# Kernel optimization log

Hardware: AMD Instinct MI355X
Metric: run time of the kernel (lower is better)

Reference implementation:

```python
import jax, jax.numpy as jnp
import numpy as np

BLOCK_SIZE = 128
FP8_MAX = 448.0
IN_FEATURES = 4096
OUT_FEATURES = 4096


def _fp8_round(x):
    # Simulate float8_e4m3fn storage; fall back to clamp-only if dtype unsupported.
    try:
        return x.astype(jnp.float8_e4m3fn).astype(jnp.float32)
    except Exception:
        return x


def setup_inputs() -> dict:
    key = jax.random.key(0)
    kx, kw = jax.random.split(key)
    x = jax.random.normal(kx, (2, 4096, IN_FEATURES), dtype=jnp.float32)
    # Kaiming-uniform-ish init, then block-quantize exactly as fp8_block_quantize does.
    bound = 1.0 / np.sqrt(IN_FEATURES)
    w = jax.random.uniform(kw, (OUT_FEATURES, IN_FEATURES), minval=-bound, maxval=bound, dtype=jnp.float32)
    w_blocks = w.reshape(-1, BLOCK_SIZE)  # (n_blocks, 128); 4096*4096 divisible by 128
    block_abs_max = jnp.maximum(jnp.max(jnp.abs(w_blocks), axis=-1), 1e-12)
    fp8_scales = block_abs_max / FP8_MAX  # (n_blocks,)
    w_scaled = jnp.clip(w_blocks / fp8_scales[:, None], -FP8_MAX, FP8_MAX)
    weight_q = _fp8_round(w_scaled).reshape(OUT_FEATURES, IN_FEATURES)
    bias = jnp.zeros((OUT_FEATURES,), dtype=jnp.float32)
    return {"x": x, "weight_q": weight_q, "fp8_scales": fp8_scales, "bias": bias}


def reference(x, weight_q, fp8_scales, bias):
    # Block-wise dequantize: flatten weight, scale each 128-element block.
    w_blocks = weight_q.reshape(-1, BLOCK_SIZE)            # (n_blocks, 128)
    w = (w_blocks * fp8_scales[:, None]).reshape(OUT_FEATURES, IN_FEATURES)
    # F.linear: y = x @ w.T + b
    return jnp.einsum('bsk,nk->bsn', x, w) + bias
```

## Files before the change

kernel.cpp:

```cpp
#include <hip/hip_runtime.h>


#define M_DIM 8192
#define N_DIM 4096
#define K_DIM 4096
#define K_TILES (K_DIM / 64)

typedef short s16x8 __attribute__((ext_vector_type(8)));
typedef float f32x4 __attribute__((ext_vector_type(4)));

__device__ __forceinline__ unsigned short f32_to_bf16(float f) {
    unsigned int u = __float_as_uint(f);
    unsigned int r = (u + 0x7fffu + ((u >> 16) & 1u)) >> 16;
    return (unsigned short)r;
}

__device__ __forceinline__ ushort4 pack4(float4 a) {
    ushort4 r;
    r.x = f32_to_bf16(a.x); r.y = f32_to_bf16(a.y);
    r.z = f32_to_bf16(a.z); r.w = f32_to_bf16(a.w);
    return r;
}

__global__ __launch_bounds__(256) void cvt_fused_kernel(
    const float4* __restrict__ x, const float4* __restrict__ wq,
    const float* __restrict__ scales,
    ushort4* __restrict__ xo, ushort4* __restrict__ wo) {
    const int b = blockIdx.x;
    const int t = threadIdx.x;
    if (b < 16384) {
        const int base = b * 512 + t;
#pragma unroll
        for (int j = 0; j < 2; ++j) {
            const int idx = base + j * 256;
            xo[idx] = pack4(x[idx]);
        }
    } else {
        const int base = (b - 16384) * 512 + t;
#pragma unroll
        for (int j = 0; j < 2; ++j) {
            const int idx = base + j * 256;
            const float s = scales[idx >> 5];
            float4 a = wq[idx];
            a.x *= s; a.y *= s; a.z *= s; a.w *= s;
            wo[idx] = pack4(a);
        }
    }
}

__device__ __forceinline__ void async_copy16(const void* g, void* l) {
    __builtin_amdgcn_global_load_lds(
        (const __attribute__((address_space(1))) unsigned int*)g,
        (__attribute__((address_space(3))) unsigned int*)l,
        16, 0, 0);
}


#define STAGE_A_HALF(h, ktt, bufb) do {                                        \
    const unsigned short* g_ = gA0 + (ktt) * 64 + (h) * (64 * K_DIM);          \
    async_copy16(g_,               ldsA + (bufb) + (h) * 8192 + aOff);         \
    async_copy16(g_ + 128 * K_DIM, ldsA + (bufb) + (h) * 8192 + 16384 + aOff); \
  } while (0)

#define STAGE_B_HALF(h, ktt, bufb) do {                                        \
    const unsigned short* g_ = gB0 + (ktt) * 64 + (h) * (32 * K_DIM);          \
    async_copy16(g_,               ldsB + (bufb) + (h) * 4096 + bOff);         \
    async_copy16(g_ + 128 * K_DIM, ldsB + (bufb) + (h) * 4096 + 16384 + bOff); \
  } while (0)

#define PHASE(qm, qn, bufb, STAGE_STMT, WAITN) do {                            \
    STAGE_STMT;                                                                \
    asm volatile("s_waitcnt vmcnt(" #WAITN ")" ::: "memory");                  \
    __builtin_amdgcn_s_barrier();                                              \
    asm volatile("" ::: "memory");                                             \
    __builtin_amdgcn_sched_barrier(0);                                         \
    s16x8 af[4][2], bf[2][2];                                                  \
    _Pragma("unroll")                                                          \
    for (int i = 0; i < 4; ++i) {                                              \
      af[i][0] = *(const s16x8*)(ldsA + (bufb) + aRowB + ((qm)*64 + i*16)*128 + kk0); \
      af[i][1] = *(const s16x8*)(ldsA + (bufb) + aRowB + ((qm)*64 + i*16)*128 + kk1); \
    }                                                                          \
    _Pragma("unroll")                                                          \
    for (int j = 0; j < 2; ++j) {                                              \
      bf[j][0] = *(const s16x8*)(ldsB + (bufb) + bRowB + ((qn)*32 + j*16)*128 + kk0); \
      bf[j][1] = *(const s16x8*)(ldsB + (bufb) + bRowB + ((qn)*32 + j*16)*128 + kk1); \
    }                                                                          \
    __builtin_amdgcn_s_setprio(1);                                             \
    _Pragma("unroll")                                                          \
    for (int i = 0; i < 4; ++i)                                                \
      _Pragma("unroll")                                                        \
      for (int j = 0; j < 2; ++j) {                                            \
        acc[(qm)*4+i][(qn)*2+j] = __builtin_amdgcn_mfma_f32_16x16x32_bf16(     \
            af[i][0], bf[j][0], acc[(qm)*4+i][(qn)*2+j], 0, 0, 0);             \
        acc[(qm)*4+i][(qn)*2+j] = __builtin_amdgcn_mfma_f32_16x16x32_bf16(     \
            af[i][1], bf[j][1], acc[(qm)*4+i][(qn)*2+j], 0, 0, 0);             \
      }                                                                        \
    __builtin_amdgcn_s_setprio(0);                                             \
  } while (0)

__global__ __launch_bounds__(512, 2) void gemm_bt_kernel(
    const unsigned short* __restrict__ A,
    const unsigned short* __restrict__ B,
    const float* __restrict__ bias,
    float* __restrict__ C)
{
    __shared__ __align__(16) char lds[131072];
    char* ldsA = lds;
    char* ldsB = lds + 32768;

    const int t = threadIdx.x;
    const int l = t & 63;
    const int w = t >> 6;
    const int wr = w >> 2;
    const int wc = w & 3;

    int id = blockIdx.x;
    id = (id & 7) * 64 + (id >> 3);
    const int m0 = (id >> 4) * 256;
    const int n0 = (id & 15) * 256;

    const int trow = t >> 3;
    const int tcol = ((t & 7) * 8) ^ ((trow & 7) * 8);
    const unsigned short* gA0 = A + (long)(m0 + trow) * K_DIM + tcol;
    const int brow = ((t >> 8) * 64) + ((t & 255) >> 3);
    const unsigned short* gB0 = B + (long)(n0 + brow) * K_DIM + tcol;
    const int aOff = t * 16;
    const int bOff = ((t >> 8) * 8192) + ((t & 255) * 16);

    const int aRowB = (wr * 128 + (l & 15)) * 128;
    const int bRowB = (wc * 64  + (l & 15)) * 128;
    const int kx  = (l >> 4) * 16;
    const int sw  = (l & 7) * 16;
    const int kk0 = kx ^ sw;
    const int kk1 = (64 + kx) ^ sw;

    f32x4 acc[8][4] = {};

    STAGE_A_HALF(0, 0, 0);
    STAGE_B_HALF(0, 0, 0);
    STAGE_B_HALF(1, 0, 0);
    STAGE_A_HALF(1, 0, 0);

    for (int kt = 0; kt < K_TILES - 1; ++kt) {
        const int cb = (kt & 1) * 65536;
        const int nb = 65536 - cb;
        PHASE(0, 0, cb, STAGE_A_HALF(0, kt + 1, nb), 6);
        PHASE(0, 1, cb, STAGE_B_HALF(0, kt + 1, nb), 6);
        PHASE(1, 0, cb, STAGE_B_HALF(1, kt + 1, nb), 6);
        PHASE(1, 1, cb, STAGE_A_HALF(1, kt + 1, nb), 6);
    }
    {
        const int cb = ((K_TILES - 1) & 1) * 65536;
        PHASE(0, 0, cb, (void)0, 4);
        PHASE(0, 1, cb, (void)0, 2);
        PHASE(1, 0, cb, (void)0, 0);
        PHASE(1, 1, cb, (void)0, 0);
    }

    const int q4 = (l >> 4) * 4;
#pragma unroll
    for (int nf = 0; nf < 4; ++nf) {
        const int col = n0 + wc * 64 + nf * 16 + (l & 15);
        const float bv = bias[col];
#pragma unroll
        for (int mf = 0; mf < 8; ++mf) {
            const long row = m0 + wr * 128 + mf * 16 + q4;
#pragma unroll
            for (int r = 0; r < 4; ++r) {
                C[(row + r) * N_DIM + col] = acc[mf][nf][r] + bv;
            }
        }
    }
}

extern "C" void kernel_launch(void* const* d_in, const int* in_sizes, int n_in,
                              void* d_out, int out_size, void* d_ws, size_t ws_size,
                              hipStream_t stream) {
    const float* x      = (const float*)d_in[0];
    const float* wq     = (const float*)d_in[1];
    const float* scales = (const float*)d_in[2];
    const float* bias   = (const float*)d_in[3];
    float* out = (float*)d_out;

    unsigned short* x_bf = (unsigned short*)d_ws;
    unsigned short* w_bf = x_bf + (size_t)M_DIM * K_DIM;

    cvt_fused_kernel<<<24576, 256, 0, stream>>>(
        (const float4*)x, (const float4*)wq, scales,
        (ushort4*)x_bf, (ushort4*)w_bf);

    gemm_bt_kernel<<<dim3(512), dim3(512), 0, stream>>>(x_bf, w_bf, bias, out);
}
```

Baseline: 510.1 us.

## Restructure GEMM k-loop into two phases and use grid-stride 16B conversion

```diff
diff --git a/kernel.cpp b/kernel.cpp
--- a/kernel.cpp
+++ b/kernel.cpp
@@ -8,42 +8,42 @@
 
 typedef short s16x8 __attribute__((ext_vector_type(8)));
 typedef float f32x4 __attribute__((ext_vector_type(4)));
-
-__device__ __forceinline__ unsigned short f32_to_bf16(float f) {
-    unsigned int u = __float_as_uint(f);
-    unsigned int r = (u + 0x7fffu + ((u >> 16) & 1u)) >> 16;
-    return (unsigned short)r;
-}
-
-__device__ __forceinline__ ushort4 pack4(float4 a) {
-    ushort4 r;
-    r.x = f32_to_bf16(a.x); r.y = f32_to_bf16(a.y);
-    r.z = f32_to_bf16(a.z); r.w = f32_to_bf16(a.w);
-    return r;
+typedef unsigned int u32x4 __attribute__((ext_vector_type(4)));
+
+__device__ __forceinline__ unsigned int pack2_bf16(float a, float b) {
+    unsigned int ua = __float_as_uint(a);
+    unsigned int ub = __float_as_uint(b);
+    unsigned int ra = ((ua + 0x7fffu + ((ua >> 16) & 1u)) >> 16) & 0xffffu;
+    unsigned int rb = (ub + 0x7fffu + ((ub >> 16) & 1u)) & 0xffff0000u;
+    return ra | rb;
 }
 
 __global__ __launch_bounds__(256) void cvt_fused_kernel(
     const float4* __restrict__ x, const float4* __restrict__ wq,
     const float* __restrict__ scales,
-    ushort4* __restrict__ xo, ushort4* __restrict__ wo) {
-    const int b = blockIdx.x;
-    const int t = threadIdx.x;
-    if (b < 16384) {
-        const int base = b * 512 + t;
-#pragma unroll
-        for (int j = 0; j < 2; ++j) {
-            const int idx = base + j * 256;
-            xo[idx] = pack4(x[idx]);
-        }
-    } else {
-        const int base = (b - 16384) * 512 + t;
-#pragma unroll
-        for (int j = 0; j < 2; ++j) {
-            const int idx = base + j * 256;
-            const float s = scales[idx >> 5];
-            float4 a = wq[idx];
+    u32x4* __restrict__ xo, u32x4* __restrict__ wo) {
+    const int NX   = (M_DIM * K_DIM) / 8;
+    const int NTOT = NX + (N_DIM * K_DIM) / 8;
+    const int stride = gridDim.x * blockDim.x;
+    for (int u = blockIdx.x * blockDim.x + threadIdx.x; u < NTOT; u += stride) {
+        if (u < NX) {
+            const float4 a = x[2 * u];
+            const float4 b = x[2 * u + 1];
+            u32x4 r;
+            r[0] = pack2_bf16(a.x, a.y); r[1] = pack2_bf16(a.z, a.w);
+            r[2] = pack2_bf16(b.x, b.y); r[3] = pack2_bf16(b.z, b.w);
+            xo[u] = r;
+        } else {
+            const int v = u - NX;
+            const float s = scales[v >> 4];
+            float4 a = wq[2 * v];
+            float4 b = wq[2 * v + 1];
             a.x *= s; a.y *= s; a.z *= s; a.w *= s;
-            wo[idx] = pack4(a);
+            b.x *= s; b.y *= s; b.z *= s; b.w *= s;
+            u32x4 r;
+            r[0] = pack2_bf16(a.x, a.y); r[1] = pack2_bf16(a.z, a.w);
+            r[2] = pack2_bf16(b.x, b.y); r[3] = pack2_bf16(b.z, b.w);
+            wo[v] = r;
         }
     }
 }
@@ -68,33 +68,41 @@
     async_copy16(g_ + 128 * K_DIM, ldsB + (bufb) + (h) * 4096 + 16384 + bOff); \
   } while (0)
 
-#define PHASE(qm, qn, bufb, STAGE_STMT, WAITN) do {                            \
-    STAGE_STMT;                                                                \
-    asm volatile("s_waitcnt vmcnt(" #WAITN ")" ::: "memory");                  \
-    __builtin_amdgcn_s_barrier();                                              \
-    asm volatile("" ::: "memory");                                             \
-    __builtin_amdgcn_sched_barrier(0);                                         \
-    s16x8 af[4][2], bf[2][2];                                                  \
+#define READ_AF(dst, qm, bufb) do {                                            \
     _Pragma("unroll")                                                          \
-    for (int i = 0; i < 4; ++i) {                                              \
-      af[i][0] = *(const s16x8*)(ldsA + (bufb) + aRowB + ((qm)*64 + i*16)*128 + kk0); \
-      af[i][1] = *(const s16x8*)(ldsA + (bufb) + aRowB + ((qm)*64 + i*16)*128 + kk1); \
+    for (int i_ = 0; i_ < 4; ++i_) {                                           \
+      dst[i_][0] = *(const s16x8*)(ldsA + (bufb) + aRowB + ((qm)*64 + i_*16)*128 + kk0); \
+      dst[i_][1] = *(const s16x8*)(ldsA + (bufb) + aRowB + ((qm)*64 + i_*16)*128 + kk1); \
     }                                                                          \
+  } while (0)
+
+#define READ_BF(dst, qn, bufb) do {                                            \
     _Pragma("unroll")                                                          \
-    for (int j = 0; j < 2; ++j) {                                              \
-      bf[j][0] = *(const s16x8*)(ldsB + (bufb) + bRowB + ((qn)*32 + j*16)*128 + kk0); \
-      bf[j][1] = *(const s16x8*)(ldsB + (bufb) + bRowB + ((qn)*32 + j*16)*128 + kk1); \
+    for (int j_ = 0; j_ < 2; ++j_) {                                           \
+      dst[j_][0] = *(const s16x8*)(ldsB + (bufb) + bRowB + ((qn)*32 + j_*16)*128 + kk0); \
+      dst[j_][1] = *(const s16x8*)(ldsB + (bufb) + bRowB + ((qn)*32 + j_*16)*128 + kk1); \
     }                                                                          \
+  } while (0)
+
+#define MFMA32(qm, AF, BX, BY) do {                                            \
     __builtin_amdgcn_s_setprio(1);                                             \
     _Pragma("unroll")                                                          \
-    for (int i = 0; i < 4; ++i)                                                \
+    for (int i_ = 0; i_ < 4; ++i_) {                                           \
       _Pragma("unroll")                                                        \
-      for (int j = 0; j < 2; ++j) {                                            \
-        acc[(qm)*4+i][(qn)*2+j] = __builtin_amdgcn_mfma_f32_16x16x32_bf16(     \
-            af[i][0], bf[j][0], acc[(qm)*4+i][(qn)*2+j], 0, 0, 0);             \
-        acc[(qm)*4+i][(qn)*2+j] = __builtin_amdgcn_mfma_f32_16x16x32_bf16(     \
-            af[i][1], bf[j][1], acc[(qm)*4+i][(qn)*2+j], 0, 0, 0);             \
+      for (int j_ = 0; j_ < 2; ++j_) {                                         \
+        acc[(qm)*4+i_][j_] = __builtin_amdgcn_mfma_f32_16x16x32_bf16(          \
+            AF[i_][0], BX[j_][0], acc[(qm)*4+i_][j_], 0, 0, 0);                \
+        acc[(qm)*4+i_][j_] = __builtin_amdgcn_mfma_f32_16x16x32_bf16(          \
+            AF[i_][1], BX[j_][1], acc[(qm)*4+i_][j_], 0, 0, 0);                \
       }                                                                        \
+      _Pragma("unroll")                                                        \
+      for (int j_ = 0; j_ < 2; ++j_) {                                         \
+        acc[(qm)*4+i_][2+j_] = __builtin_amdgcn_mfma_f32_16x16x32_bf16(        \
+            AF[i_][0], BY[j_][0], acc[(qm)*4+i_][2+j_], 0, 0, 0);              \
+        acc[(qm)*4+i_][2+j_] = __builtin_amdgcn_mfma_f32_16x16x32_bf16(        \
+            AF[i_][1], BY[j_][1], acc[(qm)*4+i_][2+j_], 0, 0, 0);              \
+      }                                                                        \
+    }                                                                          \
     __builtin_amdgcn_s_setprio(0);                                             \
   } while (0)
 
@@ -135,6 +143,7 @@
     const int kk1 = (64 + kx) ^ sw;
 
     f32x4 acc[8][4] = {};
+    s16x8 af[4][2], bfX[2][2], bfY[2][2];
 
     STAGE_A_HALF(0, 0, 0);
     STAGE_B_HALF(0, 0, 0);
@@ -144,17 +153,35 @@
     for (int kt = 0; kt < K_TILES - 1; ++kt) {
         const int cb = (kt & 1) * 65536;
         const int nb = 65536 - cb;
-        PHASE(0, 0, cb, STAGE_A_HALF(0, kt + 1, nb), 6);
-        PHASE(0, 1, cb, STAGE_B_HALF(0, kt + 1, nb), 6);
-        PHASE(1, 0, cb, STAGE_B_HALF(1, kt + 1, nb), 6);
-        PHASE(1, 1, cb, STAGE_A_HALF(1, kt + 1, nb), 6);
+        STAGE_A_HALF(0, kt + 1, nb);
+        STAGE_B_HALF(0, kt + 1, nb);
+        asm volatile("s_waitcnt vmcnt(4)" ::: "memory");
+        __builtin_amdgcn_s_barrier();
+        __builtin_amdgcn_sched_barrier(0);
+        READ_AF(af, 0, cb);
+        READ_BF(bfX, 0, cb);
+        READ_BF(bfY, 1, cb);
+        MFMA32(0, af, bfX, bfY);
+        STAGE_B_HALF(1, kt + 1, nb);
+        STAGE_A_HALF(1, kt + 1, nb);
+        __builtin_amdgcn_s_barrier();
+        __builtin_amdgcn_sched_barrier(0);
+        READ_AF(af, 1, cb);
+        MFMA32(1, af, bfX, bfY);
     }
     {
         const int cb = ((K_TILES - 1) & 1) * 65536;
-        PHASE(0, 0, cb, (void)0, 4);
-        PHASE(0, 1, cb, (void)0, 2);
-        PHASE(1, 0, cb, (void)0, 0);
-        PHASE(1, 1, cb, (void)0, 0);
+        asm volatile("s_waitcnt vmcnt(0)" ::: "memory");
+        __builtin_amdgcn_s_barrier();
+        __builtin_amdgcn_sched_barrier(0);
+        READ_AF(af, 0, cb);
+        READ_BF(bfX, 0, cb);
+        READ_BF(bfY, 1, cb);
+        MFMA32(0, af, bfX, bfY);
+        __builtin_amdgcn_s_barrier();
+        __builtin_amdgcn_sched_barrier(0);
+        READ_AF(af, 1, cb);
+        MFMA32(1, af, bfX, bfY);
     }
 
     const int q4 = (l >> 4) * 4;
@@ -185,9 +212,9 @@
     unsigned short* x_bf = (unsigned short*)d_ws;
     unsigned short* w_bf = x_bf + (size_t)M_DIM * K_DIM;
 
-    cvt_fused_kernel<<<24576, 256, 0, stream>>>(
+    cvt_fused_kernel<<<2048, 256, 0, stream>>>(
         (const float4*)x, (const float4*)wq, scales,
-        (ushort4*)x_bf, (ushort4*)w_bf);
+        (u32x4*)x_bf, (u32x4*)w_bf);
 
     gemm_bt_kernel<<<dim3(512), dim3(512), 0, stream>>>(x_bf, w_bf, bias, out);
 }
```

New measurement: 497.7 us. 2.4% less time.
